# Optimization experiments

Hardware: AMD Instinct MI355X
Metric: run time of the kernel (lower is better)

Reference implementation:

```python
import jax, jax.numpy as jnp
from jax import lax
import numpy as np

B, DIM, H, W = 1, 48, 192, 192
HEADS, K, DIL = 2, 7, 3
HD = DIM // HEADS
HID = int(DIM * 2.66)  # 127 (Restormer GEGLU hidden)
EPS = 1e-5


def _window_starts(L, Kk, D):
    # NATTEN window-start rule: keep phase i % D, shift window inside bounds.
    s = np.zeros(L, dtype=np.int32)
    for i in range(L):
        if D <= 1:
            st = max(i - Kk // 2, 0)
            if i + Kk // 2 >= L:
                st = L - Kk
        else:
            st = i - (Kk // 2) * D
            if st < 0:
                st = i % D
            elif i + (Kk // 2) * D >= L:
                imodd = i % D
                a = (L // D) * D
                b = L - a
                if imodd < b:
                    st = L - b + imodd - 2 * (Kk // 2) * D
                else:
                    st = a + imodd - Kk * D
        s[i] = st
    return s


def _nbr_tables(L, Kk, D):
    st = _window_starts(L, Kk, D)
    idx = st[:, None] + np.arange(Kk)[None, :] * D          # [L, K] absolute neighbor idx
    pb = (st - np.arange(L)) // D                            # signed offset of window start (in dilation units)
    pb = pb[:, None] + (Kk - 1) + np.arange(Kk)[None, :]     # [L, K] rpb index in [0, 2K-2]
    return jnp.asarray(idx), jnp.asarray(pb)

IH, PBH = _nbr_tables(H, K, DIL)
IW, PBW = _nbr_tables(W, K, DIL)


def layernorm(x, w, b):  # channel LN on NCHW (WithBias, biased var)
    mu = x.mean(1, keepdims=True)
    var = ((x - mu) ** 2).mean(1, keepdims=True)
    return (x - mu) / jnp.sqrt(var + EPS) * w[None, :, None, None] + b[None, :, None, None]


def na2d(x, qkv_w, qkv_b, rpb, proj_w, proj_b):
    # x: NCHW -> BHWC
    t = x.transpose(0, 2, 3, 1)
    qkv = t @ qkv_w.T + qkv_b                                # [B,H,W,3*DIM]
    qkv = qkv.reshape(B, H, W, 3, HEADS, HD)
    q, k, v = qkv[:, :, :, 0], qkv[:, :, :, 1], qkv[:, :, :, 2]
    q = q * (HD ** -0.5)
    # gather dilated 7x7 neighborhoods: [B, H, K, W, K, heads, hd]
    kn = k[:, IH[:, :, None, None], IW[None, None, :, :]]
    vn = v[:, IH[:, :, None, None], IW[None, None, :, :]]
    attn = jnp.einsum('bijnc,bixjync->bijnxy', q, kn)        # [B,H,W,heads,K,K]
    bias = rpb[:, PBH][:, :, :, PBW]                         # [heads,H,K,W,K]
    attn = attn + bias.transpose(1, 3, 0, 2, 4)
    attn = jax.nn.softmax(attn.reshape(B, H, W, HEADS, K * K), axis=-1)
    attn = attn.reshape(B, H, W, HEADS, K, K)
    out = jnp.einsum('bijnxy,bixjync->bijnc', attn, vn).reshape(B, H, W, DIM)
    out = out @ proj_w.T + proj_b
    return out.transpose(0, 3, 1, 2)


def chan_mod(x, eca_w):  # ECA-style gate: GAP -> 1D conv over channels -> sigmoid
    p = x.mean((2, 3))                                       # [B,C]
    y = lax.conv_general_dilated(p[:, None, :], eca_w[None, None, :], (1,), [(3, 3)],
                                 dimension_numbers=('NCH', 'OIH', 'NCH'))[:, 0, :]
    return jax.nn.sigmoid(y)[:, :, None, None]


def ffn(x, w_in, w_dw, w_out):  # conv-GEGLU
    t = jnp.einsum('bchw,oc->bohw', x, w_in)                 # 1x1: DIM -> 2*HID
    t = lax.conv_general_dilated(t, w_dw, (1, 1), [(1, 1), (1, 1)],
                                 feature_group_count=2 * HID,
                                 dimension_numbers=('NCHW', 'OIHW', 'NCHW'))
    x1, x2 = t[:, :HID], t[:, HID:]
    g = jax.nn.gelu(x1, approximate=False) * x2
    return jnp.einsum('bchw,oc->bohw', g, w_out)             # 1x1: HID -> DIM


def setup_inputs() -> dict:
    key = jax.random.key(0)
    ks = jax.random.split(key, 10)
    d = {
        'x': jax.random.normal(ks[0], (B, DIM, H, W), jnp.float32),
        'ln1_w': jnp.ones((DIM,), jnp.float32),
        'ln1_b': jnp.zeros((DIM,), jnp.float32),
        'qkv_w': jax.random.normal(ks[1], (3 * DIM, DIM), jnp.float32) * 0.05,
        'qkv_b': jnp.zeros((3 * DIM,), jnp.float32),
        'rpb': jax.random.normal(ks[2], (HEADS, 2 * K - 1, 2 * K - 1), jnp.float32) * 0.02,
        'proj_w': jax.random.normal(ks[3], (DIM, DIM), jnp.float32) * 0.05,
        'proj_b': jnp.zeros((DIM,), jnp.float32),
        'eca_w': jax.random.normal(ks[4], (7,), jnp.float32) * 0.1,
        'ln2_w': jnp.ones((DIM,), jnp.float32),
        'ln2_b': jnp.zeros((DIM,), jnp.float32),
        'w_in': jax.random.normal(ks[5], (2 * HID, DIM), jnp.float32) * 0.05,
        'w_dw': jax.random.normal(ks[6], (2 * HID, 1, 3, 3), jnp.float32) * 0.05,
        'w_out': jax.random.normal(ks[7], (DIM, HID), jnp.float32) * 0.05,
    }
    return d


def reference(x, ln1_w, ln1_b, qkv_w, qkv_b, rpb, proj_w, proj_b, eca_w,
              ln2_w, ln2_b, w_in, w_dw, w_out):
    xn1 = layernorm(x, ln1_w, ln1_b)
    x = x + na2d(xn1, qkv_w, qkv_b, rpb, proj_w, proj_b) * chan_mod(xn1, eca_w)
    x = x + ffn(layernorm(x, ln2_w, ln2_b), w_in, w_dw, w_out)
    return x
```

## Files before the change

kernel.cpp:

```cpp
#include <hip/hip_runtime.h>
#include <hip/hip_bf16.h>
#include <math.h>

#define HW_ (192*192)
#define Wd 192
#define HIDc 127
#define NBLK1 (HW_/32)

#define O_LN1W 0
#define O_QKVW 96
#define O_QKVB 7008
#define O_RPB  7152
#define O_PROJW 7490
#define O_PROJB 9794
#define O_ECA  9842
#define O_LN2W 9849
#define O_WIN  9945
#define O_WDW  22137
#define O_WOUT 24423
#define WTS_LEN 30519

typedef unsigned short ushort_t;

__device__ __forceinline__ float b2f(__hip_bfloat16 v){ return __bfloat162float(v); }
__device__ __forceinline__ float u2f(ushort_t h){ return __uint_as_float(((unsigned)h)<<16); }
__device__ __forceinline__ ushort_t f2u(float f){
    __hip_bfloat16 h = __float2bfloat16(f);
    union { __hip_bfloat16 b; ushort_t u; } c; c.b = h; return c.u;
}
__device__ __forceinline__ void up2(unsigned u, float& a, float& b){
    a = __uint_as_float(u << 16);
    b = __uint_as_float(u & 0xffff0000u);
}

__device__ __forceinline__ int wstart(int i){
    if (i < 9) return i % 3;
    if (i >= 183) return 171 + (i % 3);
    return i - 9;
}

__global__ void convert_kernel(
    const void* p0, const void* p1, const void* p2, const void* p3,
    const void* p4, const void* p5, const void* p6, const void* p7,
    const void* p8, const void* p9, const void* p10, const void* p11,
    const void* p12, const ushort_t* __restrict__ xu, int* __restrict__ mode_out,
    float* __restrict__ wts, ushort_t* __restrict__ qkvbf, float* __restrict__ woutT)
{
    __shared__ int sbad;
    if (threadIdx.x == 0) sbad = 0;
    __syncthreads();
    {
        unsigned u = xu[2*threadIdx.x];
        float f = __uint_as_float(u << 16);
        if (!(fabsf(f) < 100.f)) atomicAdd(&sbad, 1);
    }
    __syncthreads();
    const int md = (sbad > 16) ? 1 : 0;
    if (blockIdx.x == 0 && threadIdx.x == 0) mode_out[0] = md;

    const void* ps[13] = {p0,p1,p2,p3,p4,p5,p6,p7,p8,p9,p10,p11,p12};
    const int sz[13]  = {48,48,6912,144,338,2304,48,7,48,48,12192,2286,6096};
    const int off[13] = {O_LN1W,48,O_QKVW,O_QKVB,O_RPB,O_PROJW,O_PROJB,O_ECA,
                         O_LN2W,9897,O_WIN,O_WDW,O_WOUT};
    int b = blockIdx.x;
    if (b == 13){
        if (md){
            const float* s = (const float*)p2;
            for (int i = threadIdx.x; i < 6912; i += 256) qkvbf[i] = f2u(s[i]);
        } else {
            const ushort_t* s = (const ushort_t*)p2;
            for (int i = threadIdx.x; i < 6912; i += 256) qkvbf[i] = s[i];
        }
        return;
    }
    if (b == 14){
        if (md){
            const float* s = (const float*)p12;
            for (int i = threadIdx.x; i < 6096; i += 256){
                int c = i / 48, o = i - c*48;
                woutT[i] = s[o*127 + c];
            }
        } else {
            const __hip_bfloat16* s = (const __hip_bfloat16*)p12;
            for (int i = threadIdx.x; i < 6096; i += 256){
                int c = i / 48, o = i - c*48;
                woutT[i] = b2f(s[o*127 + c]);
            }
        }
        return;
    }
    int n = sz[b];
    float* dst = wts + off[b];
    if (md){
        const float* s = (const float*)ps[b];
        for (int i = threadIdx.x; i < n; i += 256) dst[i] = s[i];
    } else {
        const __hip_bfloat16* s = (const __hip_bfloat16*)ps[b];
        for (int i = threadIdx.x; i < n; i += 256) dst[i] = b2f(s[i]);
    }
}

__global__ __launch_bounds__(192) void ln1qkv_kernel(
    const void* __restrict__ x, const int* __restrict__ mode,
    const float* __restrict__ wts, const ushort_t* __restrict__ qkvbf,
    ushort_t* __restrict__ q, ushort_t* __restrict__ k, ushort_t* __restrict__ v,
    float* __restrict__ chpart)
{
    __shared__ ushort_t ssw[144*48];
    __shared__ float sx[32*49];
    __shared__ float sb[144];
    __shared__ float sln[96];

    const int tid = threadIdx.x;
    const int px_l = tid & 31;
    const int r6   = tid >> 5;
    const int p0   = blockIdx.x * 32;
    const int p    = p0 + px_l;

    {
        const unsigned int* srcw = (const unsigned int*)qkvbf;
        unsigned int* dstw = (unsigned int*)ssw;
        for (int i = tid; i < 3456; i += 192) dstw[i] = srcw[i];
    }
    for (int i = tid; i < 144; i += 192) sb[i] = wts[O_QKVB + i];
    for (int i = tid; i < 96;  i += 192) sln[i] = wts[O_LN1W + i];

    if (mode[0]){
        const float* xf = (const float*)x;
        for (int idx = tid; idx < 32*48; idx += 192){
            int c = idx >> 5, pl = idx & 31;
            sx[pl*49 + c] = xf[c*HW_ + p0 + pl];
        }
    } else {
        const __hip_bfloat16* xb = (const __hip_bfloat16*)x;
        for (int idx = tid; idx < 32*48; idx += 192){
            int c = idx >> 5, pl = idx & 31;
            sx[pl*49 + c] = b2f(xb[c*HW_ + p0 + pl]);
        }
    }
    __syncthreads();

    float xr[48];
    float mu = 0.f;
    #pragma unroll
    for (int c = 0; c < 48; c++){ xr[c] = sx[px_l*49 + c]; mu += xr[c]; }
    mu *= (1.f/48.f);
    float var = 0.f;
    #pragma unroll
    for (int c = 0; c < 48; c++){ float d = xr[c]-mu; var += d*d; }
    var *= (1.f/48.f);
    float rs = rsqrtf(var + 1e-5f);
    #pragma unroll
    for (int c = 0; c < 48; c++) xr[c] = (xr[c]-mu)*rs*sln[c] + sln[48+c];

    if (tid < 64){
        #pragma unroll
        for (int c = 0; c < 48; c++){
            float s = xr[c];
            s += __shfl_xor(s, 1);  s += __shfl_xor(s, 2);  s += __shfl_xor(s, 4);
            s += __shfl_xor(s, 8);  s += __shfl_xor(s, 16); s += __shfl_xor(s, 32);
            if (tid == 0) chpart[blockIdx.x*48 + c] = s * 0.5f;
        }
    }

    const int rbase = r6 * 24;
    const float scale = (r6 < 2) ? 0.20412414523193154f : 1.0f;
    float ov[24];
    #pragma unroll 4
    for (int ro = 0; ro < 24; ro++){
        int r = rbase + ro;
        float acc = sb[r];
        const uint4* wr = (const uint4*)&ssw[r*48];
        #pragma unroll
        for (int c8 = 0; c8 < 6; c8++){
            uint4 u = wr[c8];
            float f0,f1,f2,f3,f4,f5,f6,f7;
            up2(u.x,f0,f1); up2(u.y,f2,f3); up2(u.z,f4,f5); up2(u.w,f6,f7);
            acc += f0*xr[8*c8]   + f1*xr[8*c8+1] + f2*xr[8*c8+2] + f3*xr[8*c8+3]
                 + f4*xr[8*c8+4] + f5*xr[8*c8+5] + f6*xr[8*c8+6] + f7*xr[8*c8+7];
        }
        ov[ro] = acc * scale;
    }

    unsigned int pk[12];
    #pragma unroll
    for (int d = 0; d < 12; d++)
        pk[d] = (unsigned)f2u(ov[2*d]) | ((unsigned)f2u(ov[2*d+1]) << 16);
    ushort_t* tp = (r6 >> 1) == 0 ? q : ((r6 >> 1) == 1 ? k : v);
    uint4* dst4 = (uint4*)(tp + (size_t)p*48 + (r6 & 1)*24);
    dst4[0] = make_uint4(pk[0], pk[1], pk[2],  pk[3]);
    dst4[1] = make_uint4(pk[4], pk[5], pk[6],  pk[7]);
    dst4[2] = make_uint4(pk[8], pk[9], pk[10], pk[11]);
}

__global__ __launch_bounds__(256) void gatered_kernel(
    const float* __restrict__ chpart, float* __restrict__ msum)
{
    __shared__ float red[4];
    const int c = blockIdx.x;
    const int tid = threadIdx.x;
    float acc = 0.f;
    for (int b = tid; b < NBLK1; b += 256)
        acc += chpart[b*48 + c];
    acc += __shfl_xor(acc, 1);  acc += __shfl_xor(acc, 2);  acc += __shfl_xor(acc, 4);
    acc += __shfl_xor(acc, 8);  acc += __shfl_xor(acc, 16); acc += __shfl_xor(acc, 32);
    if ((tid & 63) == 0) red[tid >> 6] = acc;
    __syncthreads();
    if (tid == 0)
        msum[c] = (red[0] + red[1] + red[2] + red[3]) * (1.f / (float)HW_);
}

__global__ void gate_kernel(const float* __restrict__ msum,
                            const float* __restrict__ wts,
                            float* __restrict__ gate)
{
    __shared__ float m[48];
    int t = threadIdx.x;
    if (t < 48) m[t] = msum[t];
    __syncthreads();
    if (t < 48){
        float a = 0.f;
        for (int kk = 0; kk < 7; kk++){
            int cc = t + kk - 3;
            if (cc >= 0 && cc < 48) a += wts[O_ECA + kk] * m[cc];
        }
        gate[t] = 1.f / (1.f + expf(-a));
    }
}

__global__ __launch_bounds__(256) void attn_kernel(
    const ushort_t* __restrict__ q, const ushort_t* __restrict__ k,
    const ushort_t* __restrict__ v, const float* __restrict__ wts,
    ushort_t* __restrict__ aout)
{
    const int head = blockIdx.y;
    __shared__ float srpb[169];
    for (int i = threadIdx.x; i < 169; i += 256) srpb[i] = wts[O_RPB + head*169 + i];
    __syncthreads();

    const int tid  = threadIdx.x;
    const int px   = blockIdx.x * 128 + (tid >> 1);
    const int half = tid & 1;
    const int i = px / Wd, j = px % Wd;
    const int sti = wstart(i), stj = wstart(j);
    const int pbi = (sti - i) / 3 + 6;
    const int pbj = (stj - j) / 3 + 6;
    const int choff = head*24 + half*12;

    float qr[12];
    {
        const ushort4* qp = (const ushort4*)(q + (size_t)px*48 + choff);
        #pragma unroll
        for (int b = 0; b < 3; b++){
            ushort4 uu = qp[b];
            qr[4*b]   = u2f(uu.x); qr[4*b+1] = u2f(uu.y);
            qr[4*b+2] = u2f(uu.z); qr[4*b+3] = u2f(uu.w);
        }
    }

    float m = -1e30f, s = 0.f;
    float acc[12];
    #pragma unroll
    for (int c = 0; c < 12; c++) acc[c] = 0.f;

    #pragma unroll
    for (int xx = 0; xx < 7; xx++){
        int ii = sti + 3*xx;
        #pragma unroll
        for (int yy = 0; yy < 7; yy++){
            int jj = stj + 3*yy;
            const size_t nb = (size_t)(ii*Wd + jj)*48 + choff;
            const ushort4* kp = (const ushort4*)(k + nb);
            const ushort4* vp = (const ushort4*)(v + nb);
            ushort4 k0 = kp[0], k1 = kp[1], k2 = kp[2];
            ushort4 v0 = vp[0], v1 = vp[1], v2 = vp[2];
            float d = qr[0]*u2f(k0.x) + qr[1]*u2f(k0.y)
                    + qr[2]*u2f(k0.z) + qr[3]*u2f(k0.w)
                    + qr[4]*u2f(k1.x) + qr[5]*u2f(k1.y)
                    + qr[6]*u2f(k1.z) + qr[7]*u2f(k1.w)
                    + qr[8]*u2f(k2.x) + qr[9]*u2f(k2.y)
                    + qr[10]*u2f(k2.z) + qr[11]*u2f(k2.w);
            d += __shfl_xor(d, 1);
            float sc = d + srpb[(pbi+xx)*13 + (pbj+yy)];
            float mn = fmaxf(m, sc);
            float corr = __expf(m - mn);
            float p = __expf(sc - mn);
            s = s*corr + p;
            m = mn;
            acc[0]  = acc[0] *corr + p*u2f(v0.x);
            acc[1]  = acc[1] *corr + p*u2f(v0.y);
            acc[2]  = acc[2] *corr + p*u2f(v0.z);
            acc[3]  = acc[3] *corr + p*u2f(v0.w);
            acc[4]  = acc[4] *corr + p*u2f(v1.x);
            acc[5]  = acc[5] *corr + p*u2f(v1.y);
            acc[6]  = acc[6] *corr + p*u2f(v1.z);
            acc[7]  = acc[7] *corr + p*u2f(v1.w);
            acc[8]  = acc[8] *corr + p*u2f(v2.x);
            acc[9]  = acc[9] *corr + p*u2f(v2.y);
            acc[10] = acc[10]*corr + p*u2f(v2.z);
            acc[11] = acc[11]*corr + p*u2f(v2.w);
        }
    }
    const float inv = 1.f / s;
    #pragma unroll
    for (int c = 0; c < 12; c++)
        aout[(size_t)(choff + c)*HW_ + px] = f2u(acc[c] * inv);
}

__global__ __launch_bounds__(256) void proj_kernel(
    const ushort_t* __restrict__ aout, const float* __restrict__ wts,
    const float* __restrict__ gate, const void* __restrict__ x,
    const int* __restrict__ mode, float* __restrict__ x2)
{
    const int tid = threadIdx.x;
    const int px = blockIdx.x * 64 + (tid & 63);
    const int og = tid >> 6;
    const int ob = og * 12;

    float ar[48];
    #pragma unroll
    for (int c = 0; c < 48; c++) ar[c] = u2f(aout[(size_t)c*HW_ + px]);

    const float* xf = (const float*)x;
    const __hip_bfloat16* xb = (const __hip_bfloat16*)x;
    const int md = mode[0];
    #pragma unroll 2
    for (int oo = 0; oo < 12; oo++){
        int o = ob + oo;
        float acc = wts[O_PROJB + o];
        const float4* swr = (const float4*)&wts[O_PROJW + o*48];
        #pragma unroll
        for (int c4 = 0; c4 < 12; c4++){
            float4 w = swr[c4];
            acc += w.x*ar[4*c4] + w.y*ar[4*c4+1] + w.z*ar[4*c4+2] + w.w*ar[4*c4+3];
        }
        float res = md ? xf[o*HW_ + px] : b2f(xb[o*HW_ + px]);
        x2[o*HW_ + px] = res + acc * gate[o];
    }
}

__global__ __launch_bounds__(128) void pw1_kernel(
    const float* __restrict__ x2, const float* __restrict__ wts,
    ushort_t* __restrict__ t)
{
    int ob   = blockIdx.y * 64;
    int ocnt = min(64, 254 - ob);

    int p = blockIdx.x * 128 + threadIdx.x;
    float xr[48];
    float mu = 0.f;
    #pragma unroll
    for (int c = 0; c < 48; c++){ xr[c] = x2[c*HW_ + p]; mu += xr[c]; }
    mu *= (1.f/48.f);
    float var = 0.f;
    #pragma unroll
    for (int c = 0; c < 48; c++){ float d = xr[c]-mu; var += d*d; }
    var *= (1.f/48.f);
    float rs = rsqrtf(var + 1e-5f);
    #pragma unroll
    for (int c = 0; c < 48; c++)
        xr[c] = (xr[c]-mu)*rs*wts[O_LN2W + c] + wts[O_LN2W + 48 + c];

    for (int o = 0; o < ocnt; o++){
        float acc = 0.f;
        const float4* swr = (const float4*)&wts[O_WIN + (ob+o)*48];
        #pragma unroll
        for (int c4 = 0; c4 < 12; c4++){
            float4 w = swr[c4];
            acc += w.x*xr[4*c4] + w.y*xr[4*c4+1] + w.z*xr[4*c4+2] + w.w*xr[4*c4+3];
        }
        t[(ob+o)*HW_ + p] = f2u(acc);
    }
}

__global__ __launch_bounds__(256) void dw_kernel(
    const ushort_t* __restrict__ t, const float* __restrict__ wts,
    ushort_t* __restrict__ g)
{
    int ch = blockIdx.y;
    int p  = blockIdx.x * 256 + threadIdx.x;
    int i  = p / Wd, j = p % Wd;
    float w1[9], w2[9];
    #pragma unroll
    for (int s = 0; s < 9; s++){
        w1[s] = wts[O_WDW + ch*9 + s];
        w2[s] = wts[O_WDW + (ch+HIDc)*9 + s];
    }
    const ushort_t* t1 = t + (size_t)ch * HW_;
    const ushort_t* t2 = t + (size_t)(ch+HIDc) * HW_;
    float a1 = 0.f, a2 = 0.f;
    #pragma unroll
    for (int di = 0; di < 3; di++){
        int ii = i + di - 1;
        if (ii < 0 || ii >= 192) continue;
        #pragma unroll
        for (int dj = 0; dj < 3; dj++){
            int jj = j + dj - 1;
            if (jj < 0 || jj >= 192) continue;
            int off = ii*Wd + jj;
            a1 += w1[di*3+dj]*u2f(t1[off]);
            a2 += w2[di*3+dj]*u2f(t2[off]);
        }
    }
    float ge = a1 * 0.5f * (1.f + erff(a1 * 0.70710678118654752f));
    g[(size_t)ch*HW_ + p] = f2u(ge * a2);
}

__global__ __launch_bounds__(128) void pw2_kernel(
    const ushort_t* __restrict__ g, const float* __restrict__ woutT,
    const float* __restrict__ x2, void* __restrict__ outv,
    const int* __restrict__ mode)
{
    const int ob = blockIdx.y * 24;
    const int p  = blockIdx.x * 128 + threadIdx.x;
    float acc[24];
    #pragma unroll
    for (int o = 0; o < 24; o++) acc[o] = 0.f;
    #pragma unroll 4
    for (int c = 0; c < 127; c++){
        float gv = u2f(g[(size_t)c*HW_ + p]);
        const float* wr = woutT + c*48 + ob;
        #pragma unroll
        for (int o = 0; o < 24; o++) acc[o] += wr[o]*gv;
    }
    if (mode[0]){
        float* out = (float*)outv;
        #pragma unroll
        for (int o = 0; o < 24; o++){
            int oc = ob + o;
            out[(size_t)oc*HW_ + p] = x2[(size_t)oc*HW_ + p] + acc[o];
        }
    } else {
        __hip_bfloat16* out = (__hip_bfloat16*)outv;
        #pragma unroll
        for (int o = 0; o < 24; o++){
            int oc = ob + o;
            out[(size_t)oc*HW_ + p] =
                __float2bfloat16(x2[(size_t)oc*HW_ + p] + acc[o]);
        }
    }
}

extern "C" void kernel_launch(void* const* d_in, const int* in_sizes, int n_in,
                              void* d_out, int out_size, void* d_ws, size_t ws_size,
                              hipStream_t stream)
{
    (void)in_sizes; (void)n_in; (void)out_size;

    char* ws = (char*)d_ws;
    ushort_t* q    = (ushort_t*)(ws);
    ushort_t* k    = (ushort_t*)(ws + 3538944);
    ushort_t* v    = (ushort_t*)(ws + 7077888);
    ushort_t* aout = (ushort_t*)(ws + 10616832);
    ushort_t* t    = (ushort_t*)(ws);
    float*    x2   = (float*)   (ws + 18726912);
    ushort_t* g    = (ushort_t*)(ws + 25804800);
    float*    gate = (float*)   (ws + 35168448);
    int*      mode = (int*)     (ws + 35168640);
    float*    wts  = (float*)   (ws + 35168656);
    float*    chpart=(float*)   (ws + 35168656 + (size_t)WTS_LEN*4);
    float*    msum = chpart + (size_t)NBLK1*48;
    ushort_t* qkvbf= (ushort_t*)(msum + 48);
    float*    woutT= (float*)(qkvbf + 6912);

    size_t need = 35168656 + (size_t)WTS_LEN*4 + (size_t)NBLK1*48*4 + 48*4
                + 6912*2 + 6096*4;
    if (ws_size < need) return;

    convert_kernel<<<15, 256, 0, stream>>>(
        d_in[1], d_in[2], d_in[3], d_in[4], d_in[5], d_in[6], d_in[7],
        d_in[8], d_in[9], d_in[10], d_in[11], d_in[12], d_in[13],
        (const ushort_t*)d_in[0], mode, wts, qkvbf, woutT);

    ln1qkv_kernel<<<dim3(NBLK1), 192, 0, stream>>>(d_in[0], mode, wts, qkvbf,
                                                   q, k, v, chpart);
    gatered_kernel<<<48, 256, 0, stream>>>(chpart, msum);
    gate_kernel<<<1, 64, 0, stream>>>(msum, wts, gate);
    attn_kernel<<<dim3(HW_/128, 2), 256, 0, stream>>>(q, k, v, wts, aout);
    proj_kernel<<<dim3(HW_/64), 256, 0, stream>>>(aout, wts, gate, d_in[0],
                                                  mode, x2);
    pw1_kernel<<<dim3(HW_/128, 4), 128, 0, stream>>>(x2, wts, t);
    dw_kernel<<<dim3(HW_/256, 127), 256, 0, stream>>>(t, wts, g);
    pw2_kernel<<<dim3(HW_/128, 2), 128, 0, stream>>>(g, woutT, x2, d_out, mode);
}
```

Measured before the change: 283.0 us.

## Fuse projection with LN2 and first pointwise conv; widen LN1/QKV blocks

```diff
diff --git a/kernel.cpp b/kernel.cpp
--- a/kernel.cpp
+++ b/kernel.cpp
@@ -5,7 +5,7 @@
 #define HW_ (192*192)
 #define Wd 192
 #define HIDc 127
-#define NBLK1 (HW_/32)
+#define NBLK1 (HW_/64)
 
 #define O_LN1W 0
 #define O_QKVW 96
@@ -100,41 +100,30 @@
     }
 }
 
-__global__ __launch_bounds__(192) void ln1qkv_kernel(
+__global__ __launch_bounds__(384) void ln1qkv_kernel(
     const void* __restrict__ x, const int* __restrict__ mode,
     const float* __restrict__ wts, const ushort_t* __restrict__ qkvbf,
     ushort_t* __restrict__ q, ushort_t* __restrict__ k, ushort_t* __restrict__ v,
     float* __restrict__ chpart)
 {
-    __shared__ ushort_t ssw[144*48];
-    __shared__ float sx[32*49];
-    __shared__ float sb[144];
-    __shared__ float sln[96];
-
-    const int tid = threadIdx.x;
-    const int px_l = tid & 31;
-    const int r6   = tid >> 5;
-    const int p0   = blockIdx.x * 32;
+    __shared__ float sx[64*49];
+
+    const int tid  = threadIdx.x;
+    const int px_l = tid & 63;
+    const int r6   = __builtin_amdgcn_readfirstlane(tid >> 6);
+    const int p0   = blockIdx.x * 64;
     const int p    = p0 + px_l;
-
-    {
-        const unsigned int* srcw = (const unsigned int*)qkvbf;
-        unsigned int* dstw = (unsigned int*)ssw;
-        for (int i = tid; i < 3456; i += 192) dstw[i] = srcw[i];
-    }
-    for (int i = tid; i < 144; i += 192) sb[i] = wts[O_QKVB + i];
-    for (int i = tid; i < 96;  i += 192) sln[i] = wts[O_LN1W + i];
 
     if (mode[0]){
         const float* xf = (const float*)x;
-        for (int idx = tid; idx < 32*48; idx += 192){
-            int c = idx >> 5, pl = idx & 31;
+        for (int idx = tid; idx < 64*48; idx += 384){
+            int c = idx >> 6, pl = idx & 63;
             sx[pl*49 + c] = xf[c*HW_ + p0 + pl];
         }
     } else {
         const __hip_bfloat16* xb = (const __hip_bfloat16*)x;
-        for (int idx = tid; idx < 32*48; idx += 192){
-            int c = idx >> 5, pl = idx & 31;
+        for (int idx = tid; idx < 64*48; idx += 384){
+            int c = idx >> 6, pl = idx & 63;
             sx[pl*49 + c] = b2f(xb[c*HW_ + p0 + pl]);
         }
     }
@@ -151,7 +140,8 @@
     var *= (1.f/48.f);
     float rs = rsqrtf(var + 1e-5f);
     #pragma unroll
-    for (int c = 0; c < 48; c++) xr[c] = (xr[c]-mu)*rs*sln[c] + sln[48+c];
+    for (int c = 0; c < 48; c++)
+        xr[c] = (xr[c]-mu)*rs*wts[O_LN1W + c] + wts[O_LN1W + 48 + c];
 
     if (tid < 64){
         #pragma unroll
@@ -159,7 +149,7 @@
             float s = xr[c];
             s += __shfl_xor(s, 1);  s += __shfl_xor(s, 2);  s += __shfl_xor(s, 4);
             s += __shfl_xor(s, 8);  s += __shfl_xor(s, 16); s += __shfl_xor(s, 32);
-            if (tid == 0) chpart[blockIdx.x*48 + c] = s * 0.5f;
+            if (tid == 0) chpart[blockIdx.x*48 + c] = s;
         }
     }
 
@@ -169,8 +159,8 @@
     #pragma unroll 4
     for (int ro = 0; ro < 24; ro++){
         int r = rbase + ro;
-        float acc = sb[r];
-        const uint4* wr = (const uint4*)&ssw[r*48];
+        float acc = wts[O_QKVB + r];
+        const uint4* wr = (const uint4*)(qkvbf + r*48);
         #pragma unroll
         for (int c8 = 0; c8 < 6; c8++){
             uint4 u = wr[c8];
@@ -307,23 +297,35 @@
         aout[(size_t)(choff + c)*HW_ + px] = f2u(acc[c] * inv);
 }
 
-__global__ __launch_bounds__(256) void proj_kernel(
+__global__ __launch_bounds__(256) void projpw1_kernel(
     const ushort_t* __restrict__ aout, const float* __restrict__ wts,
     const float* __restrict__ gate, const void* __restrict__ x,
-    const int* __restrict__ mode, float* __restrict__ x2)
-{
-    const int tid = threadIdx.x;
-    const int px = blockIdx.x * 64 + (tid & 63);
-    const int og = tid >> 6;
-    const int ob = og * 12;
+    const int* __restrict__ mode, float* __restrict__ x2,
+    ushort_t* __restrict__ t)
+{
+    __shared__ float saout[64*49];
+    __shared__ float sx2[64*49];
+
+    const int tid  = threadIdx.x;
+    const int px_l = tid & 63;
+    const int og   = __builtin_amdgcn_readfirstlane(tid >> 6);
+    const int px0  = blockIdx.x * 64;
+    const int px   = px0 + px_l;
+
+    for (int idx = tid; idx < 64*48; idx += 256){
+        int c = idx >> 6, pl = idx & 63;
+        saout[pl*49 + c] = u2f(aout[(size_t)c*HW_ + px0 + pl]);
+    }
+    __syncthreads();
 
     float ar[48];
     #pragma unroll
-    for (int c = 0; c < 48; c++) ar[c] = u2f(aout[(size_t)c*HW_ + px]);
+    for (int c = 0; c < 48; c++) ar[c] = saout[px_l*49 + c];
 
     const float* xf = (const float*)x;
     const __hip_bfloat16* xb = (const __hip_bfloat16*)x;
     const int md = mode[0];
+    const int ob = og * 12;
     #pragma unroll 2
     for (int oo = 0; oo < 12; oo++){
         int o = ob + oo;
@@ -335,22 +337,16 @@
             acc += w.x*ar[4*c4] + w.y*ar[4*c4+1] + w.z*ar[4*c4+2] + w.w*ar[4*c4+3];
         }
         float res = md ? xf[o*HW_ + px] : b2f(xb[o*HW_ + px]);
-        x2[o*HW_ + px] = res + acc * gate[o];
-    }
-}
-
-__global__ __launch_bounds__(128) void pw1_kernel(
-    const float* __restrict__ x2, const float* __restrict__ wts,
-    ushort_t* __restrict__ t)
-{
-    int ob   = blockIdx.y * 64;
-    int ocnt = min(64, 254 - ob);
-
-    int p = blockIdx.x * 128 + threadIdx.x;
+        float val = res + acc * gate[o];
+        x2[o*HW_ + px] = val;
+        sx2[px_l*49 + o] = val;
+    }
+    __syncthreads();
+
     float xr[48];
     float mu = 0.f;
     #pragma unroll
-    for (int c = 0; c < 48; c++){ xr[c] = x2[c*HW_ + p]; mu += xr[c]; }
+    for (int c = 0; c < 48; c++){ xr[c] = sx2[px_l*49 + c]; mu += xr[c]; }
     mu *= (1.f/48.f);
     float var = 0.f;
     #pragma unroll
@@ -361,15 +357,18 @@
     for (int c = 0; c < 48; c++)
         xr[c] = (xr[c]-mu)*rs*wts[O_LN2W + c] + wts[O_LN2W + 48 + c];
 
-    for (int o = 0; o < ocnt; o++){
+    const int o20 = og * 64;
+    for (int t2 = 0; t2 < 64; t2++){
+        int o2 = o20 + t2;
+        if (o2 >= 254) break;
         float acc = 0.f;
-        const float4* swr = (const float4*)&wts[O_WIN + (ob+o)*48];
+        const float4* swr = (const float4*)&wts[O_WIN + o2*48];
         #pragma unroll
         for (int c4 = 0; c4 < 12; c4++){
             float4 w = swr[c4];
             acc += w.x*xr[4*c4] + w.y*xr[4*c4+1] + w.z*xr[4*c4+2] + w.w*xr[4*c4+3];
         }
-        t[(ob+o)*HW_ + p] = f2u(acc);
+        t[(size_t)o2*HW_ + px] = f2u(acc);
     }
 }
 
@@ -472,14 +471,13 @@
         d_in[8], d_in[9], d_in[10], d_in[11], d_in[12], d_in[13],
         (const ushort_t*)d_in[0], mode, wts, qkvbf, woutT);
 
-    ln1qkv_kernel<<<dim3(NBLK1), 192, 0, stream>>>(d_in[0], mode, wts, qkvbf,
+    ln1qkv_kernel<<<dim3(NBLK1), 384, 0, stream>>>(d_in[0], mode, wts, qkvbf,
                                                    q, k, v, chpart);
     gatered_kernel<<<48, 256, 0, stream>>>(chpart, msum);
     gate_kernel<<<1, 64, 0, stream>>>(msum, wts, gate);
     attn_kernel<<<dim3(HW_/128, 2), 256, 0, stream>>>(q, k, v, wts, aout);
-    proj_kernel<<<dim3(HW_/64), 256, 0, stream>>>(aout, wts, gate, d_in[0],
-                                                  mode, x2);
-    pw1_kernel<<<dim3(HW_/128, 4), 128, 0, stream>>>(x2, wts, t);
+    projpw1_kernel<<<dim3(HW_/64), 256, 0, stream>>>(aout, wts, gate, d_in[0],
+                                                     mode, x2, t);
     dw_kernel<<<dim3(HW_/256, 127), 256, 0, stream>>>(t, wts, g);
     pw2_kernel<<<dim3(HW_/128, 2), 128, 0, stream>>>(g, woutT, x2, d_out, mode);
 }
```

Result: faster. 272.1 us (-3.8%).
